# Performance work log

Hardware: AMD Instinct MI355X
Metric: run time of the kernel (lower is better)

Reference implementation:

```python
import jax, jax.numpy as jnp
import numpy as np

B, T, D = 4, 2048, 1024

def layer_norm(x, gamma, bias):
    # NOTE: faithfully reproduces the source's (buggy) LN: x - mu/sqrt(var), unbiased var
    mu = jnp.mean(x, axis=-1, keepdims=True)
    var = jnp.var(x, axis=-1, ddof=1, keepdims=True)
    return (x - mu / jnp.sqrt(var)) * gamma + bias

def setup_inputs() -> dict:
    key = jax.random.key(0)
    ks = jax.random.split(key, 8)
    scale = 1.0 / np.sqrt(D)
    return {
        'x': jax.random.normal(ks[0], (B, T, D), dtype=jnp.float32),
        'gamma1': jnp.ones((D,), jnp.float32),
        'beta1': jnp.zeros((D,), jnp.float32),
        'w_q': jax.random.uniform(ks[1], (D, D), jnp.float32, -scale, scale),
        'w_k': jax.random.uniform(ks[2], (D, D), jnp.float32, -scale, scale),
        'w_v': jax.random.uniform(ks[3], (D, D), jnp.float32, -scale, scale),
        'gamma2': jnp.ones((D,), jnp.float32),
        'beta2': jnp.zeros((D,), jnp.float32),
        'W1': jax.random.uniform(ks[4], (D, D), jnp.float32, -scale, scale),
        'b1': jnp.zeros((D,), jnp.float32),
        'W2': jax.random.uniform(ks[5], (D, D), jnp.float32, -scale, scale),
        'b2': jnp.zeros((D,), jnp.float32),
    }

def reference(x, gamma1, beta1, w_q, w_k, w_v, gamma2, beta2, W1, b1, W2, b2):
    d_model = x.shape[-1]
    t = x.shape[1]
    h = layer_norm(x, gamma1, beta1)
    q = jnp.einsum('btk,kd->btd', h, w_q)
    k = jnp.einsum('btk,kd->btd', h, w_k)
    v = jnp.einsum('btk,kd->btd', h, w_v)
    scale = 1.0 / jnp.sqrt(jnp.asarray(d_model, x.dtype))
    causal = jnp.tril(jnp.ones((t, t), dtype=bool))
    mask = jnp.where(causal, 0.0, -jnp.inf).astype(x.dtype)
    scores = jnp.einsum('bqd,bkd->bqk', q, k) * scale + mask
    attn = jax.nn.softmax(scores, axis=-1)
    y = jnp.einsum('bqt,btd->bqd', attn, v) + x
    h2 = layer_norm(y, gamma2, beta2)
    out = jnp.maximum(h2 @ W1 + b1, 0.0) @ W2 + b2
    return out + y
```

## Files before the change

kernel.cpp:

```cpp
#include <hip/hip_runtime.h>
#include <hip/hip_bf16.h>
#include <math.h>

using bf16 = __hip_bfloat16;

static constexpr int Bn = 4;
static constexpr int Tn = 2048;
static constexpr int Dn = 1024;

typedef __attribute__((ext_vector_type(8))) short bf16x8;
typedef __attribute__((ext_vector_type(4))) float f32x4;

__device__ __forceinline__ float ldf(float v) { return v; }
__device__ __forceinline__ float ldf(bf16 v) { return __bfloat162float(v); }
__device__ __forceinline__ bf16 f2b(float v) { return __float2bfloat16(v); }
__device__ __forceinline__ float b2f(short s) {
    return __uint_as_float(((unsigned)(unsigned short)s) << 16);
}
__device__ __forceinline__ short f2bs(float v) {
    bf16 t = __float2bfloat16(v);
    return *reinterpret_cast<short*>(&t);
}

template <typename T> __device__ __forceinline__ T from_float(float v);
template <> __device__ __forceinline__ float from_float<float>(float v) { return v; }
template <> __device__ __forceinline__ bf16 from_float<bf16>(float v) { return f2b(v); }

__device__ __forceinline__ void load4(const float* p, float* v) {
    const float4 t = *(const float4*)p;
    v[0] = t.x; v[1] = t.y; v[2] = t.z; v[3] = t.w;
}
__device__ __forceinline__ void load4(const bf16* p, float* v) {
    const short4 t = *(const short4*)p;
    v[0] = b2f(t.x); v[1] = b2f(t.y); v[2] = b2f(t.z); v[3] = b2f(t.w);
}

__device__ __forceinline__ void async_copy16(const bf16* g, bf16* l) {
    __builtin_amdgcn_global_load_lds(
        (const __attribute__((address_space(1))) void*)g,
        (__attribute__((address_space(3))) void*)l,
        16, 0, 0);
}

template <int BM, int BN, int MINW, typename OutT, typename ResT, bool RELU, bool VSPLIT>
__global__ __launch_bounds__(256, MINW) void gemm_nt(
    const bf16* __restrict__ A, const bf16* __restrict__ Bm,
    OutT* __restrict__ C, const float* __restrict__ bias,
    const ResT* __restrict__ res, bf16* __restrict__ vtp,
    int M, int N, int K, int lda, int ldb, int ldc,
    long sA, long sB, long sC, long sR, int mode)
{
    const int bm = blockIdx.y, bn = blockIdx.x, bz = blockIdx.z;
    if (mode == 1 && bn * BN > bm * BM + (BM - 1)) return;
    const int kend = bm * BM + BM;
    const int kmax = (mode == 2) ? (kend < K ? kend : K) : K;

    const bf16* Ab = A + (size_t)bz * sA;
    const bf16* Bb = Bm + (size_t)bz * sB;

    constexpr int WROWS = BM / 64;
    constexpr int WCOLS = 4 / WROWS;
    constexpr int TM = 64;
    constexpr int TN = BN / WCOLS;
    constexpr int MT = TM / 16;
    constexpr int NT = TN / 16;
    constexpr int nA = BM / 16;
    constexpr int nB = BN / 16;

    __shared__ __align__(16) bf16 As[2 * BM * 32];
    __shared__ __align__(16) bf16 Bs[2 * BN * 32];

    const int tid = threadIdx.x;
    const int wave = tid >> 6;
    const int lane = tid & 63;
    const int wm = wave / WCOLS;
    const int wn = wave % WCOLS;

    f32x4 acc[MT][NT] = {};

    const int lr = lane >> 2;
    const int lc = (lane & 3) * 8;
    const bf16* gAc[nA / 4]; bf16* lAc[nA / 4];
    const bf16* gBc[nB / 4]; bf16* lBc[nB / 4];
#pragma unroll
    for (int i = 0; i < nA / 4; ++i) {
        const int c = wave + 4 * i;
        gAc[i] = Ab + (size_t)(bm * BM + c * 16 + lr) * lda + lc;
        lAc[i] = &As[c * 512];
    }
#pragma unroll
    for (int i = 0; i < nB / 4; ++i) {
        const int c = wave + 4 * i;
        gBc[i] = Bb + (size_t)(bn * BN + c * 16 + lr) * ldb + lc;
        lBc[i] = &Bs[c * 512];
    }

    const int arow = lane & 15;
    const int kq = (lane >> 4) * 8;

    for (int k0 = 0; k0 < kmax; k0 += 64) {
#pragma unroll
        for (int hh = 0; hh < 2; ++hh) {
#pragma unroll
            for (int i = 0; i < nA / 4; ++i)
                async_copy16(gAc[i] + k0 + 32 * hh, lAc[i] + hh * (BM * 32));
#pragma unroll
            for (int i = 0; i < nB / 4; ++i)
                async_copy16(gBc[i] + k0 + 32 * hh, lBc[i] + hh * (BN * 32));
        }
        __syncthreads();

#pragma unroll
        for (int hh = 0; hh < 2; ++hh) {
            const bf16* Ah = As + hh * (BM * 32);
            const bf16* Bh = Bs + hh * (BN * 32);
            bf16x8 af[MT], bfm[NT];
#pragma unroll
            for (int t = 0; t < MT; ++t)
                af[t] = *(const bf16x8*)&Ah[(wm * TM + t * 16 + arow) * 32 + kq];
#pragma unroll
            for (int t = 0; t < NT; ++t)
                bfm[t] = *(const bf16x8*)&Bh[(wn * TN + t * 16 + arow) * 32 + kq];
#pragma unroll
            for (int mt = 0; mt < MT; ++mt)
#pragma unroll
                for (int nt = 0; nt < NT; ++nt)
                    acc[mt][nt] = __builtin_amdgcn_mfma_f32_16x16x32_bf16(
                        af[mt], bfm[nt], acc[mt][nt], 0, 0, 0);
        }
        __syncthreads();
    }

    const int rowBase = bm * BM + wm * TM;
    const int colBase = bn * BN + wn * TN;
    const int qrow = (lane >> 4) * 4;
    const int ccol = lane & 15;

    if (VSPLIT && bn * BN >= 2048) {
#pragma unroll
        for (int mt = 0; mt < MT; ++mt) {
            const int t0 = rowBase + mt * 16 + qrow;
            const int b = t0 >> 11, t = t0 & (Tn - 1);
            bf16* vb = vtp + (size_t)b * Dn * Tn + t;
#pragma unroll
            for (int nt = 0; nt < NT; ++nt) {
                const int d = colBase + nt * 16 + ccol - 2048;
                short4 o;
                o.x = f2bs(acc[mt][nt][0]);
                o.y = f2bs(acc[mt][nt][1]);
                o.z = f2bs(acc[mt][nt][2]);
                o.w = f2bs(acc[mt][nt][3]);
                *(short4*)(vb + (size_t)d * Tn) = o;
            }
        }
        return;
    }

    OutT* Cb = C + (size_t)bz * sC;
    const ResT* Rb = res ? (res + (size_t)bz * sR) : nullptr;
#pragma unroll
    for (int mt = 0; mt < MT; ++mt) {
#pragma unroll
        for (int nt = 0; nt < NT; ++nt) {
            const int cc = colBase + nt * 16 + ccol;
            const float bv = bias ? bias[cc] : 0.0f;
#pragma unroll
            for (int r = 0; r < 4; ++r) {
                const int rr = rowBase + mt * 16 + qrow + r;
                float v = acc[mt][nt][r] + bv;
                if (RELU) v = fmaxf(v, 0.0f);
                if (Rb) v += ldf(Rb[(size_t)rr * ldc + cc]);
                Cb[(size_t)rr * ldc + cc] = from_float<OutT>(v);
            }
        }
    }
}

template <typename InT>
__global__ __launch_bounds__(256) void ln_kernel(
    const InT* __restrict__ x, const float* __restrict__ gamma,
    const float* __restrict__ beta, bf16* __restrict__ out)
{
    const int row = blockIdx.x;
    const int tid = threadIdx.x;
    const int j = tid * 4;
    const InT* xr = x + (size_t)row * Dn;

    float v[4];
    load4(xr + j, v);
    float s = v[0] + v[1] + v[2] + v[3];
    float sq = v[0] * v[0] + v[1] * v[1] + v[2] * v[2] + v[3] * v[3];
#pragma unroll
    for (int o = 32; o > 0; o >>= 1) {
        s += __shfl_down(s, o);
        sq += __shfl_down(sq, o);
    }
    __shared__ float red[2][4];
    const int lane = tid & 63, w = tid >> 6;
    if (lane == 0) { red[0][w] = s; red[1][w] = sq; }
    __syncthreads();
    s  = red[0][0] + red[0][1] + red[0][2] + red[0][3];
    sq = red[1][0] + red[1][1] + red[1][2] + red[1][3];
    const float mean = s / (float)Dn;
    const float var = (sq - s * s / (float)Dn) / (float)(Dn - 1);
    const float coef = mean * rsqrtf(var);

    const float4 g = *(const float4*)(gamma + j);
    const float4 be = *(const float4*)(beta + j);
    short4 o;
    o.x = f2bs((v[0] - coef) * g.x + be.x);
    o.y = f2bs((v[1] - coef) * g.y + be.y);
    o.z = f2bs((v[2] - coef) * g.z + be.z);
    o.w = f2bs((v[3] - coef) * g.w + be.w);
    *(short4*)(out + (size_t)row * Dn + j) = o;
}

__global__ __launch_bounds__(256) void softmax_kernel(
    const bf16* __restrict__ S, bf16* __restrict__ P)
{
    const int r = blockIdx.x;
    const int b = r >> 11, i = r & (Tn - 1);
    const bf16* srow = S + ((size_t)b * Tn + i) * Tn;
    bf16* prow = P + ((size_t)b * Tn + i) * Tn;
    const int L = i + 1;
    const float scale = 0.03125f;
    const int tid = threadIdx.x;
    const int j0 = tid * 8;
    const int lane = tid & 63, w = tid >> 6;

    float v[8];
    if (j0 < L) {
        const bf16x8 sv = *(const bf16x8*)(srow + j0);
#pragma unroll
        for (int e = 0; e < 8; ++e)
            v[e] = (j0 + e < L) ? b2f(sv[e]) * scale : -INFINITY;
    } else {
#pragma unroll
        for (int e = 0; e < 8; ++e) v[e] = -INFINITY;
    }

    float mx = v[0];
#pragma unroll
    for (int e = 1; e < 8; ++e) mx = fmaxf(mx, v[e]);
#pragma unroll
    for (int o = 32; o > 0; o >>= 1) mx = fmaxf(mx, __shfl_down(mx, o));
    __shared__ float rmx[4], rsum[4];
    if (lane == 0) rmx[w] = mx;
    __syncthreads();
    mx = fmaxf(fmaxf(rmx[0], rmx[1]), fmaxf(rmx[2], rmx[3]));

    float p[8], sum = 0.f;
#pragma unroll
    for (int e = 0; e < 8; ++e) { p[e] = __expf(v[e] - mx); sum += p[e]; }
#pragma unroll
    for (int o = 32; o > 0; o >>= 1) sum += __shfl_down(sum, o);
    if (lane == 0) rsum[w] = sum;
    __syncthreads();
    sum = rsum[0] + rsum[1] + rsum[2] + rsum[3];
    const float inv = 1.0f / sum;

    bf16x8 pv;
#pragma unroll
    for (int e = 0; e < 8; ++e) pv[e] = f2bs(p[e] * inv);
    *(bf16x8*)(prow + j0) = pv;
}

struct WPtrs { const float* p[5]; };

__global__ __launch_bounds__(256) void wtrans_kernel(WPtrs wp, bf16* __restrict__ dst)
{
    __shared__ bf16 tile[32][33];
    const int z = blockIdx.z;
    const float* src = wp.p[z];
    bf16* d = dst + (size_t)z * Dn * Dn;
    const int c0 = blockIdx.x * 32, r0 = blockIdx.y * 32;
    const int tx = threadIdx.x & 31;
    const int ty = threadIdx.x >> 5;
#pragma unroll
    for (int dy = 0; dy < 32; dy += 8)
        tile[ty + dy][tx] = f2b(src[(size_t)(r0 + ty + dy) * Dn + (c0 + tx)]);
    __syncthreads();
#pragma unroll
    for (int dy = 0; dy < 32; dy += 8)
        d[(size_t)(c0 + ty + dy) * Dn + (r0 + tx)] = tile[tx][ty + dy];
}

extern "C" void kernel_launch(void* const* d_in, const int* in_sizes, int n_in,
                              void* d_out, int out_size, void* d_ws, size_t ws_size,
                              hipStream_t stream) {
    const float* x      = (const float*)d_in[0];
    const float* gamma1 = (const float*)d_in[1];
    const float* beta1  = (const float*)d_in[2];
    const float* w_q    = (const float*)d_in[3];
    const float* w_k    = (const float*)d_in[4];
    const float* w_v    = (const float*)d_in[5];
    const float* gamma2 = (const float*)d_in[6];
    const float* beta2  = (const float*)d_in[7];
    const float* W1     = (const float*)d_in[8];
    const float* b1     = (const float*)d_in[9];
    const float* W2     = (const float*)d_in[10];
    const float* b2     = (const float*)d_in[11];
    float* out = (float*)d_out;

    char* ws = (char*)d_ws;
    size_t off = 0;
    auto alloc = [&](size_t bytes) {
        char* p = ws + off;
        off += (bytes + 255) & ~(size_t)255;
        return p;
    };
    const size_t BT = (size_t)Bn * Tn;
    bf16* h    = (bf16*)alloc(BT * Dn * 2);
    bf16* qk   = (bf16*)alloc(BT * 2 * Dn * 2);
    bf16* vt   = (bf16*)alloc(BT * Dn * 2);
    bf16* wbuf = (bf16*)alloc((size_t)5 * Dn * Dn * 2);
    bf16* S    = (bf16*)alloc((size_t)Bn * Tn * Tn * 2);
    bf16* P    = (bf16*)alloc((size_t)Bn * Tn * Tn * 2);
    bf16* y    = S;
    bf16* h2   = h;
    bf16* mid  = qk;

    const dim3 blk(256);
    const long TD  = (long)Tn * Dn;
    const long TT  = (long)Tn * Tn;
    const long TD2 = (long)Tn * 2 * Dn;

    WPtrs wp; wp.p[0] = w_q; wp.p[1] = w_k; wp.p[2] = w_v; wp.p[3] = W1; wp.p[4] = W2;
    wtrans_kernel<<<dim3(32, 32, 5), blk, 0, stream>>>(wp, wbuf);

    ln_kernel<float><<<dim3((unsigned)BT), blk, 0, stream>>>(x, gamma1, beta1, h);

    gemm_nt<128, 128, 4, bf16, float, false, true><<<dim3(24, 64, 1), blk, 0, stream>>>(
        h, wbuf, qk, nullptr, nullptr, vt,
        (int)BT, 3 * Dn, Dn, Dn, Dn, 2 * Dn, 0, 0, 0, 0, 0);

    gemm_nt<128, 128, 4, bf16, float, false, false><<<dim3(16, 16, Bn), blk, 0, stream>>>(
        qk, qk + 1024, S, nullptr, nullptr, nullptr,
        Tn, Tn, Dn, 2 * Dn, 2 * Dn, Tn, TD2, TD2, TT, 0, 1);

    softmax_kernel<<<dim3((unsigned)BT), blk, 0, stream>>>(S, P);

    gemm_nt<128, 128, 4, bf16, float, false, false><<<dim3(8, 16, Bn), blk, 0, stream>>>(
        P, vt, y, nullptr, x, nullptr,
        Tn, Dn, Tn, Tn, Tn, Dn, TT, TD, TD, TD, 2);

    ln_kernel<bf16><<<dim3((unsigned)BT), blk, 0, stream>>>(y, gamma2, beta2, h2);

    gemm_nt<128, 128, 4, bf16, float, true, false><<<dim3(8, 64, 1), blk, 0, stream>>>(
        h2, wbuf + (size_t)3 * Dn * Dn, mid, b1, nullptr, nullptr,
        (int)BT, Dn, Dn, Dn, Dn, Dn, 0, 0, 0, 0, 0);

    gemm_nt<128, 128, 4, float, bf16, false, false><<<dim3(8, 64, 1), blk, 0, stream>>>(
        mid, wbuf + (size_t)4 * Dn * Dn, out, b2, y, nullptr,
        (int)BT, Dn, Dn, Dn, Dn, Dn, 0, 0, 0, 0, 0);
}
```

Measured before the change: 363.6 us.

## Fuse softmax into QK and PV GEMMs, stage V transpose through LDS

Removes the separate softmax kernel and the P buffer. The QK^T GEMM epilogue now writes exp(scale*s) with the causal mask applied. The PV GEMM accumulates row sums of the bf16 probabilities from its A fragments and divides by them in its epilogue. The V-transpose epilogue of the QKV GEMM is restaged through shared memory so the transposed writes to global memory are coalesced. The unnormalised exp skips max subtraction, which relies on scores being small; larger scores risk overflow or precision loss.

```diff
diff --git a/kernel.cpp b/kernel.cpp
--- a/kernel.cpp
+++ b/kernel.cpp
@@ -42,7 +42,7 @@
         16, 0, 0);
 }
 
-template <int BM, int BN, int MINW, typename OutT, typename ResT, bool RELU, bool VSPLIT>
+template <int BM, int BN, int MINW, int EPI, typename OutT, typename ResT, bool RELU>
 __global__ __launch_bounds__(256, MINW) void gemm_nt(
     const bf16* __restrict__ A, const bf16* __restrict__ Bm,
     OutT* __restrict__ C, const float* __restrict__ bias,
@@ -66,9 +66,13 @@
     constexpr int NT = TN / 16;
     constexpr int nA = BM / 16;
     constexpr int nB = BN / 16;
-
-    __shared__ __align__(16) bf16 As[2 * BM * 32];
-    __shared__ __align__(16) bf16 Bs[2 * BN * 32];
+    constexpr int TSTR = 132;
+    constexpr int SME = (EPI == 1) ? (BM * TSTR) : (2 * (BM + BN) * 32);
+
+    __shared__ __align__(16) bf16 smem[SME];
+    __shared__ float rs[(EPI == 3) ? BM : 1];
+    bf16* As = smem;
+    bf16* Bs = smem + 2 * BM * 32;
 
     const int tid = threadIdx.x;
     const int wave = tid >> 6;
@@ -77,6 +81,7 @@
     const int wn = wave % WCOLS;
 
     f32x4 acc[MT][NT] = {};
+    float rsum[MT] = {};
 
     const int lr = lane >> 2;
     const int lc = (lane & 3) * 8;
@@ -121,6 +126,12 @@
 #pragma unroll
             for (int t = 0; t < NT; ++t)
                 bfm[t] = *(const bf16x8*)&Bh[(wn * TN + t * 16 + arow) * 32 + kq];
+            if (EPI == 3 && wn == 0) {
+#pragma unroll
+                for (int t = 0; t < MT; ++t)
+#pragma unroll
+                    for (int e = 0; e < 8; ++e) rsum[t] += b2f(af[t][e]);
+            }
 #pragma unroll
             for (int mt = 0; mt < MT; ++mt)
 #pragma unroll
@@ -136,21 +147,61 @@
     const int qrow = (lane >> 4) * 4;
     const int ccol = lane & 15;
 
-    if (VSPLIT && bn * BN >= 2048) {
+    if (EPI == 3) {
+#pragma unroll
+        for (int t = 0; t < MT; ++t) {
+            float v = rsum[t];
+            v += __shfl_xor(v, 16);
+            v += __shfl_xor(v, 32);
+            if (wn == 0 && lane < 16) rs[wm * TM + t * 16 + lane] = v;
+        }
+        __syncthreads();
+    }
+
+    if (EPI == 1 && bn * BN >= 2048) {
+        bf16* tt = smem;
 #pragma unroll
         for (int mt = 0; mt < MT; ++mt) {
-            const int t0 = rowBase + mt * 16 + qrow;
-            const int b = t0 >> 11, t = t0 & (Tn - 1);
-            bf16* vb = vtp + (size_t)b * Dn * Tn + t;
+            const int tl = wm * TM + mt * 16 + qrow;
 #pragma unroll
             for (int nt = 0; nt < NT; ++nt) {
-                const int d = colBase + nt * 16 + ccol - 2048;
+                const int dl = wn * TN + nt * 16 + ccol;
                 short4 o;
                 o.x = f2bs(acc[mt][nt][0]);
                 o.y = f2bs(acc[mt][nt][1]);
                 o.z = f2bs(acc[mt][nt][2]);
                 o.w = f2bs(acc[mt][nt][3]);
-                *(short4*)(vb + (size_t)d * Tn) = o;
+                *(short4*)&tt[dl * TSTR + tl] = o;
+            }
+        }
+        __syncthreads();
+        const int dl = tid >> 1;
+        const int th = (tid & 1) * 64;
+        const int dg = bn * BN - 2048 + dl;
+        const int b = (bm * BM) >> 11;
+        const int tin = (bm * BM) & (Tn - 1);
+        bf16* dst = vtp + ((size_t)b * Dn + dg) * Tn + tin + th;
+        const bf16* srcl = &tt[dl * TSTR + th];
+#pragma unroll
+        for (int i = 0; i < 16; ++i)
+            ((short4*)dst)[i] = ((const short4*)srcl)[i];
+        return;
+    }
+
+    if (EPI == 2) {
+        OutT* Cb = C + (size_t)bz * sC;
+        const float scale = 0.03125f;
+#pragma unroll
+        for (int mt = 0; mt < MT; ++mt) {
+#pragma unroll
+            for (int nt = 0; nt < NT; ++nt) {
+                const int cc = colBase + nt * 16 + ccol;
+#pragma unroll
+                for (int r = 0; r < 4; ++r) {
+                    const int rr = rowBase + mt * 16 + qrow + r;
+                    const float e = (cc <= rr) ? __expf(acc[mt][nt][r] * scale) : 0.0f;
+                    Cb[(size_t)rr * ldc + cc] = from_float<OutT>(e);
+                }
             }
         }
         return;
@@ -160,6 +211,12 @@
     const ResT* Rb = res ? (res + (size_t)bz * sR) : nullptr;
 #pragma unroll
     for (int mt = 0; mt < MT; ++mt) {
+        float inv4[4];
+        if (EPI == 3) {
+#pragma unroll
+            for (int r = 0; r < 4; ++r)
+                inv4[r] = 1.0f / rs[wm * TM + mt * 16 + qrow + r];
+        }
 #pragma unroll
         for (int nt = 0; nt < NT; ++nt) {
             const int cc = colBase + nt * 16 + ccol;
@@ -167,7 +224,9 @@
 #pragma unroll
             for (int r = 0; r < 4; ++r) {
                 const int rr = rowBase + mt * 16 + qrow + r;
-                float v = acc[mt][nt][r] + bv;
+                float v = acc[mt][nt][r];
+                if (EPI == 3) v *= inv4[r];
+                v += bv;
                 if (RELU) v = fmaxf(v, 0.0f);
                 if (Rb) v += ldf(Rb[(size_t)rr * ldc + cc]);
                 Cb[(size_t)rr * ldc + cc] = from_float<OutT>(v);
@@ -213,56 +272,6 @@
     o.z = f2bs((v[2] - coef) * g.z + be.z);
     o.w = f2bs((v[3] - coef) * g.w + be.w);
     *(short4*)(out + (size_t)row * Dn + j) = o;
-}
-
-__global__ __launch_bounds__(256) void softmax_kernel(
-    const bf16* __restrict__ S, bf16* __restrict__ P)
-{
-    const int r = blockIdx.x;
-    const int b = r >> 11, i = r & (Tn - 1);
-    const bf16* srow = S + ((size_t)b * Tn + i) * Tn;
-    bf16* prow = P + ((size_t)b * Tn + i) * Tn;
-    const int L = i + 1;
-    const float scale = 0.03125f;
-    const int tid = threadIdx.x;
-    const int j0 = tid * 8;
-    const int lane = tid & 63, w = tid >> 6;
-
-    float v[8];
-    if (j0 < L) {
-        const bf16x8 sv = *(const bf16x8*)(srow + j0);
-#pragma unroll
-        for (int e = 0; e < 8; ++e)
-            v[e] = (j0 + e < L) ? b2f(sv[e]) * scale : -INFINITY;
-    } else {
-#pragma unroll
-        for (int e = 0; e < 8; ++e) v[e] = -INFINITY;
-    }
-
-    float mx = v[0];
-#pragma unroll
-    for (int e = 1; e < 8; ++e) mx = fmaxf(mx, v[e]);
-#pragma unroll
-    for (int o = 32; o > 0; o >>= 1) mx = fmaxf(mx, __shfl_down(mx, o));
-    __shared__ float rmx[4], rsum[4];
-    if (lane == 0) rmx[w] = mx;
-    __syncthreads();
-    mx = fmaxf(fmaxf(rmx[0], rmx[1]), fmaxf(rmx[2], rmx[3]));
-
-    float p[8], sum = 0.f;
-#pragma unroll
-    for (int e = 0; e < 8; ++e) { p[e] = __expf(v[e] - mx); sum += p[e]; }
-#pragma unroll
-    for (int o = 32; o > 0; o >>= 1) sum += __shfl_down(sum, o);
-    if (lane == 0) rsum[w] = sum;
-    __syncthreads();
-    sum = rsum[0] + rsum[1] + rsum[2] + rsum[3];
-    const float inv = 1.0f / sum;
-
-    bf16x8 pv;
-#pragma unroll
-    for (int e = 0; e < 8; ++e) pv[e] = f2bs(p[e] * inv);
-    *(bf16x8*)(prow + j0) = pv;
 }
 
 struct WPtrs { const float* p[5]; };
@@ -315,8 +324,7 @@
     bf16* vt   = (bf16*)alloc(BT * Dn * 2);
     bf16* wbuf = (bf16*)alloc((size_t)5 * Dn * Dn * 2);
     bf16* S    = (bf16*)alloc((size_t)Bn * Tn * Tn * 2);
-    bf16* P    = (bf16*)alloc((size_t)Bn * Tn * Tn * 2);
-    bf16* y    = S;
+    bf16* y    = (bf16*)alloc(BT * Dn * 2);
     bf16* h2   = h;
     bf16* mid  = qk;
 
@@ -330,27 +338,25 @@
 
     ln_kernel<float><<<dim3((unsigned)BT), blk, 0, stream>>>(x, gamma1, beta1, h);
 
-    gemm_nt<128, 128, 4, bf16, float, false, true><<<dim3(24, 64, 1), blk, 0, stream>>>(
+    gemm_nt<128, 128, 4, 1, bf16, float, false><<<dim3(24, 64, 1), blk, 0, stream>>>(
         h, wbuf, qk, nullptr, nullptr, vt,
         (int)BT, 3 * Dn, Dn, Dn, Dn, 2 * Dn, 0, 0, 0, 0, 0);
 
-    gemm_nt<128, 128, 4, bf16, float, false, false><<<dim3(16, 16, Bn), blk, 0, stream>>>(
+    gemm_nt<128, 128, 4, 2, bf16, float, false><<<dim3(16, 16, Bn), blk, 0, stream>>>(
         qk, qk + 1024, S, nullptr, nullptr, nullptr,
         Tn, Tn, Dn, 2 * Dn, 2 * Dn, Tn, TD2, TD2, TT, 0, 1);
 
-    softmax_kernel<<<dim3((unsigned)BT), blk, 0, stream>>>(S, P);
-
-    gemm_nt<128, 128, 4, bf16, float, false, false><<<dim3(8, 16, Bn), blk, 0, stream>>>(
-        P, vt, y, nullptr, x, nullptr,
+    gemm_nt<128, 128, 4, 3, bf16, float, false><<<dim3(8, 16, Bn), blk, 0, stream>>>(
+        S, vt, y, nullptr, x, nullptr,
         Tn, Dn, Tn, Tn, Tn, Dn, TT, TD, TD, TD, 2);
 
     ln_kernel<bf16><<<dim3((unsigned)BT), blk, 0, stream>>>(y, gamma2, beta2, h2);
 
-    gemm_nt<128, 128, 4, bf16, float, true, false><<<dim3(8, 64, 1), blk, 0, stream>>>(
+    gemm_nt<128, 128, 4, 0, bf16, float, true><<<dim3(8, 64, 1), blk, 0, stream>>>(
         h2, wbuf + (size_t)3 * Dn * Dn, mid, b1, nullptr, nullptr,
         (int)BT, Dn, Dn, Dn, Dn, Dn, 0, 0, 0, 0, 0);
 
-    gemm_nt<128, 128, 4, float, bf16, false, false><<<dim3(8, 64, 1), blk, 0, stream>>>(
+    gemm_nt<128, 128, 4, 0, float, bf16, false><<<dim3(8, 64, 1), blk, 0, stream>>>(
         mid, wbuf + (size_t)4 * Dn * Dn, out, b2, y, nullptr,
         (int)BT, Dn, Dn, Dn, Dn, Dn, 0, 0, 0, 0, 0);
 }
```

Result: no change. 363.5 us (-0.0%).
